# Performance work log

Hardware: AMD Instinct MI355X
Metric: run time of the kernel (lower is better)

Reference implementation:

```python
import jax, jax.numpy as jnp
import numpy as np

B, L, H = 512, 10, 256   # batch dialogs, max context len (=dia_len), hidden_size
D = 2 * H                # utt encoding dim (bidirectional)
E = 0.01                 # self.e
BN_EPS = 1e-5


def _linear(x, w, b):
    return x @ w.T + b


def _bn(x, g, b):
    # BatchNorm2d over channel dim 1 of [B, L, L, hid]; training-mode batch stats.
    m = jnp.mean(x, axis=(0, 2, 3), keepdims=True)
    v = jnp.mean((x - m) ** 2, axis=(0, 2, 3), keepdims=True)
    return (x - m) / jnp.sqrt(v + BN_EPS) * g[None, :, None, None] + b[None, :, None, None]


def setup_inputs() -> dict:
    key = jax.random.key(0)
    ks = jax.random.split(key, 24)
    u = lambda k, s: jax.random.uniform(k, s, jnp.float32, -0.02, 0.02)
    n = lambda k, s: jax.random.normal(k, s, jnp.float32) * 0.05
    inp = {
        'utt_encs': jax.random.normal(ks[0], (B, L, D), jnp.float32),
        'aij_eps': jax.random.normal(ks[1], (B, L, L), jnp.float32),
        'sij_eps': jax.random.normal(ks[2], (B, L, L), jnp.float32),
        'context_lens': jax.random.randint(ks[3], (B,), 2, L + 1),
        # mlp_aij_mij: Linear(4H->H), BN, ReLU, Linear(H->H), BN, ReLU, Linear(H->1)
        'a_w1': u(ks[4], (H, 2 * D)), 'a_b1': jnp.zeros((H,)),
        'a_g1': jnp.ones((L,)), 'a_be1': jnp.zeros((L,)),
        'a_w2': u(ks[5], (H, H)), 'a_b2': jnp.zeros((H,)),
        'a_g2': jnp.ones((L,)), 'a_be2': jnp.zeros((L,)),
        'a_w3': u(ks[6], (1, H)), 'a_b3': jnp.zeros((1,)),
        # mlp_sij: Linear(4H->H), BN, Tanh, Linear(H->H), BN, Tanh
        's_w1': u(ks[7], (H, 2 * D)), 's_b1': jnp.zeros((H,)),
        's_g1': jnp.ones((L,)), 's_be1': jnp.zeros((L,)),
        's_w2': u(ks[8], (H, H)), 's_b2': jnp.zeros((H,)),
        's_g2': jnp.ones((L,)), 's_be2': jnp.zeros((L,)),
        'mu_w': u(ks[9], (1, H)), 'mu_b': jnp.zeros((1,)),
        'sg_w': u(ks[10], (1, H)), 'sg_b': jnp.zeros((1,)),
        # update_hidden_state: GRU(2H -> H), single step
        'gru_wi': n(ks[11], (3 * H, D)), 'gru_wh': n(ks[12], (3 * H, H)),
        'gru_bi': jnp.zeros((3 * H,)), 'gru_bh': jnp.zeros((3 * H,)),
    }
    return inp


def reference(utt_encs, aij_eps, sij_eps, context_lens,
              a_w1, a_b1, a_g1, a_be1, a_w2, a_b2, a_g2, a_be2, a_w3, a_b3,
              s_w1, s_b1, s_g1, s_be1, s_w2, s_b2, s_g2, s_be2,
              mu_w, mu_b, sg_w, sg_b, gru_wi, gru_wh, gru_bi, gru_bh):
    # pairwise concat [B, L, L, 4H]
    x_ij = jnp.concatenate([
        jnp.broadcast_to(utt_encs[:, :, None, :], (B, L, L, D)),
        jnp.broadcast_to(utt_encs[:, None, :, :], (B, L, L, D)),
    ], axis=-1)
    # aij branch
    h1 = jax.nn.relu(_bn(_linear(x_ij, a_w1, a_b1), a_g1, a_be1))
    h2 = jax.nn.relu(_bn(_linear(h1, a_w2, a_b2), a_g2, a_be2))
    aij_mij = _linear(h2, a_w3, a_b3)[..., 0]                      # [B, L, L]
    aij_mu = jax.nn.softplus(aij_mij) + E
    aij_std = jnp.sqrt(jax.nn.softplus((1.0 - aij_mu) * aij_mu) + E)
    aij = jax.nn.softplus(aij_eps * aij_std + aij_mu) + E
    # sij branch
    t1 = jnp.tanh(_bn(_linear(x_ij, s_w1, s_b1), s_g1, s_be1))
    sij_latent = jnp.tanh(_bn(_linear(t1, s_w2, s_b2), s_g2, s_be2))
    sij_mu = _linear(sij_latent, mu_w, mu_b)[..., 0]
    sij_sigma = _linear(sij_latent, sg_w, sg_b)[..., 0]
    sij = sij_eps * jnp.sqrt(aij * sij_sigma * sij_sigma) + aij * sij_mu
    wij = aij * sij                                                # [B, L, L]
    # per-dialog aggregation (vectorized): anchor = context_lens - 1,
    # neighbors are j < anchor (anchor row, anchor excluded, j <= num_neighbours)
    anchor = context_lens - 1                                      # [B]
    w_row = jnp.take_along_axis(wij, anchor[:, None, None], axis=1)[:, 0, :]  # [B, L]
    mask = jnp.arange(L)[None, :] < anchor[:, None]
    logits = jnp.where(mask, w_row, -jnp.inf)
    p = jax.nn.softmax(logits, axis=-1)
    p = jnp.where(mask, p, 0.0)
    message = jnp.einsum('bj,bjd->bd', p, utt_encs)                # [B, 2H]
    ue_a = jnp.take_along_axis(utt_encs, anchor[:, None, None], axis=1)[:, 0, :]
    h0 = ue_a[:, :H] + ue_a[:, H:]                                 # [B, H]
    # single GRU step (torch GRU cell math)
    gi = message @ gru_wi.T + gru_bi
    gh = h0 @ gru_wh.T + gru_bh
    i_r, i_z, i_n = jnp.split(gi, 3, axis=-1)
    h_r, h_z, h_n = jnp.split(gh, 3, axis=-1)
    r = jax.nn.sigmoid(i_r + h_r)
    z = jax.nn.sigmoid(i_z + h_z)
    ncand = jnp.tanh(i_n + r * h_n)
    return (1.0 - z) * ncand + z * h0                              # [B, H]
```

## Files before the change

kernel.cpp:

```cpp
#include <hip/hip_runtime.h>
#include <math.h>


typedef __attribute__((ext_vector_type(8))) short short8;
typedef __attribute__((ext_vector_type(4))) float f32x4;

__device__ __forceinline__ float softplusf(float x) {
  return x > 0.f ? x + log1pf(expf(-x)) : log1pf(expf(x));
}
__device__ __forceinline__ float wred64(float v) {
#pragma unroll
  for (int o = 32; o > 0; o >>= 1) v += __shfl_down(v, o);
  return v;
}
__device__ __forceinline__ unsigned short f2bf(float f) {
  unsigned int u = __float_as_uint(f);
  u += 0x7fffu + ((u >> 16) & 1u);
  return (unsigned short)(u >> 16);
}
__device__ __forceinline__ float bf2f(unsigned short u) {
  return __uint_as_float(((unsigned int)u) << 16);
}
__device__ __forceinline__ float tanh_fast(float x) {
  float ex = __expf(2.f * x);
  return 1.f - 2.f / (ex + 1.f);
}
__device__ __forceinline__ float sigmoid_fast(float x) {
  return 1.f / (1.f + __expf(-x));
}
__device__ __forceinline__ short8 pack8(const float* __restrict__ p) {
  float4 v0 = *(const float4*)p;
  float4 v1 = *(const float4*)(p + 4);
  short8 r;
  r[0] = (short)f2bf(v0.x); r[1] = (short)f2bf(v0.y);
  r[2] = (short)f2bf(v0.z); r[3] = (short)f2bf(v0.w);
  r[4] = (short)f2bf(v1.x); r[5] = (short)f2bf(v1.y);
  r[6] = (short)f2bf(v1.z); r[7] = (short)f2bf(v1.w);
  return r;
}

__global__ __launch_bounds__(256) void prep_weights(
    const float* __restrict__ utt,
    const float* __restrict__ a_w1, const float* __restrict__ s_w1,
    const float* __restrict__ a_w2, const float* __restrict__ s_w2,
    const float* __restrict__ gru_wi, const float* __restrict__ gru_wh,
    unsigned short* __restrict__ Af, unsigned short* __restrict__ Bf,
    unsigned short* __restrict__ W2fa, unsigned short* __restrict__ W2fs,
    unsigned short* __restrict__ wibf, unsigned short* __restrict__ whbf) {
  int i = blockIdx.x * 256 + threadIdx.x;
  if (i < 327680) {
    int lane = i & 63, ks = (i >> 6) & 15, rb = i >> 10;
    int row = rb * 16 + (lane & 15);
    int k = ks * 32 + (lane >> 4) * 8;
    *(short8*)&Af[i * 8] = pack8(&utt[row * 512 + k]);
    return;
  }
  i -= 327680;
  if (i < 65536) {
    int lane = i & 63, cf = (i >> 6) & 3, ks = (i >> 8) & 15, cb = i >> 12;
    int c = cb * 64 + cf * 16 + (lane & 15);
    int k = ks * 32 + (lane >> 4) * 8;
    const float* src;
    if (c < 256)       src = &a_w1[c * 1024 + k];
    else if (c < 512)  src = &a_w1[(c - 256) * 1024 + 512 + k];
    else if (c < 768)  src = &s_w1[(c - 512) * 1024 + k];
    else               src = &s_w1[(c - 768) * 1024 + 512 + k];
    *(short8*)&Bf[i * 8] = pack8(src);
    return;
  }
  i -= 65536;
  if (i < 8192) {
    int lane = i & 63, cf = (i >> 6) & 3, ks = (i >> 8) & 7, cb = i >> 11;
    int c = cb * 64 + cf * 16 + (lane & 15);
    int k = ks * 32 + (lane >> 4) * 8;
    *(short8*)&W2fa[i * 8] = pack8(&a_w2[c * 256 + k]);
    return;
  }
  i -= 8192;
  if (i < 8192) {
    int lane = i & 63, cf = (i >> 6) & 3, ks = (i >> 8) & 7, cb = i >> 11;
    int c = cb * 64 + cf * 16 + (lane & 15);
    int k = ks * 32 + (lane >> 4) * 8;
    *(short8*)&W2fs[i * 8] = pack8(&s_w2[c * 256 + k]);
    return;
  }
  i -= 8192;
  if (i < 49152) { *(short8*)&wibf[i * 8] = pack8(&gru_wi[i * 8]); return; }
  i -= 49152;
  *(short8*)&whbf[i * 8] = pack8(&gru_wh[i * 8]);
}

__global__ __launch_bounds__(256) void gemm_pq_swz(
    const unsigned short* __restrict__ Af, const unsigned short* __restrict__ Bf,
    unsigned short* __restrict__ C) {
  int t = threadIdx.x;
  int w = t >> 6, l = t & 63, li = l & 15, lg = l >> 4;
  int rb0 = blockIdx.x * 4;
  int cb = blockIdx.y * 4 + w;
  const unsigned short* Bb = Bf + cb * (16 * 4 * 512);
  f32x4 acc[4][4] = {};
  short8 acur[4], bcur[4], anxt[4], bnxt[4];
#pragma unroll
  for (int fr = 0; fr < 4; ++fr) acur[fr] = *(const short8*)&Af[((rb0 + fr) * 16 + 0) * 512 + l * 8];
#pragma unroll
  for (int cf = 0; cf < 4; ++cf) bcur[cf] = *(const short8*)&Bb[(0 * 4 + cf) * 512 + l * 8];
  for (int ks = 0; ks < 16; ++ks) {
    if (ks < 15) {
#pragma unroll
      for (int fr = 0; fr < 4; ++fr) anxt[fr] = *(const short8*)&Af[((rb0 + fr) * 16 + ks + 1) * 512 + l * 8];
#pragma unroll
      for (int cf = 0; cf < 4; ++cf) bnxt[cf] = *(const short8*)&Bb[((ks + 1) * 4 + cf) * 512 + l * 8];
    }
#pragma unroll
    for (int fr = 0; fr < 4; ++fr)
#pragma unroll
      for (int cf = 0; cf < 4; ++cf)
        acc[fr][cf] = __builtin_amdgcn_mfma_f32_16x16x32_bf16(acur[fr], bcur[cf], acc[fr][cf], 0, 0, 0);
#pragma unroll
    for (int fr = 0; fr < 4; ++fr) acur[fr] = anxt[fr];
#pragma unroll
    for (int cf = 0; cf < 4; ++cf) bcur[cf] = bnxt[cf];
  }
  int rowBase = blockIdx.x * 64, colBase = cb * 64;
#pragma unroll
  for (int fr = 0; fr < 4; ++fr)
#pragma unroll
    for (int reg = 0; reg < 4; ++reg) {
      int r = rowBase + fr * 16 + lg * 4 + reg;
      unsigned short* crow = C + r * 1024 + colBase + li;
#pragma unroll
      for (int cf = 0; cf < 4; ++cf) crow[cf * 16] = f2bf(acc[fr][cf][reg]);
    }
}

__global__ __launch_bounds__(256) void stats_kernel(
    const unsigned short* __restrict__ PQ, const float* __restrict__ a_b1,
    const float* __restrict__ s_b1, float* __restrict__ Part) {
  __shared__ float lbins[4][32];
  int b = blockIdx.x, t = threadIdx.x;
  int w = t >> 6, l = t & 63;
  int half = t >> 7;
  int tt = t & 127;
  int c0 = tt * 2;
  int p_off = half ? 512 : 0;
  const unsigned short* base = PQ + b * 10240 + p_off;
  const float* b1 = half ? s_b1 : a_b1;
  float Q0[10], Q1[10];
#pragma unroll
  for (int j = 0; j < 10; ++j) {
    unsigned int qq = *(const unsigned int*)&base[j * 1024 + 256 + c0];
    Q0[j] = bf2f((unsigned short)qq);
    Q1[j] = bf2f((unsigned short)(qq >> 16));
  }
  float sq = 0.f, sq2 = 0.f, qb0 = 0.f, qb1 = 0.f;
#pragma unroll
  for (int j = 0; j < 10; ++j) {
    sq += Q0[j] + Q1[j];
    sq2 += Q0[j] * Q0[j] + Q1[j] * Q1[j];
    qb0 += Q0[j];
    qb1 += Q1[j];
  }
  qb0 *= 0.1f;
  qb1 *= 0.1f;
  float b10 = b1[c0], b11 = b1[c0 + 1];
  float r;
  r = wred64(sq);  if (l == 0) lbins[w][0] = r;
  r = wred64(sq2); if (l == 0) lbins[w][1] = r;
#pragma unroll
  for (int i = 0; i < 10; ++i) {
    unsigned int pp = *(const unsigned int*)&base[i * 1024 + c0];
    float P0 = bf2f((unsigned short)pp);
    float P1 = bf2f((unsigned short)(pp >> 16));
    float a0 = P0 + b10, a1 = P1 + b11;
    r = wred64(P0 + P1);                 if (l == 0) lbins[w][2 + i * 3] = r;
    r = wred64(a0 * a0 + a1 * a1);       if (l == 0) lbins[w][3 + i * 3] = r;
    r = wred64(a0 * qb0 + a1 * qb1);     if (l == 0) lbins[w][4 + i * 3] = r;
  }
  __syncthreads();
  if (t < 64) {
    int br = t >> 5, s = t & 31;
    Part[(b * 2 + br) * 32 + s] = lbins[br * 2][s] + lbins[br * 2 + 1][s];
  }
}

__global__ void reduce_bn1(const float* __restrict__ Part,
                           const float* __restrict__ a_b1, const float* __restrict__ s_b1,
                           const float* __restrict__ a_g1, const float* __restrict__ a_be1,
                           const float* __restrict__ s_g1, const float* __restrict__ s_be1,
                           float* __restrict__ ST) {
  __shared__ float tmp[256];
  __shared__ float mom[32];
  int br = blockIdx.x, t = threadIdx.x;
  int v = t & 31, c = t >> 5;
  float s = 0.f;
  for (int b = c * 64; b < c * 64 + 64; ++b) s += Part[(b * 2 + br) * 32 + v];
  tmp[t] = s;
  __syncthreads();
  if (t < 32) {
    float m = 0.f;
#pragma unroll
    for (int k = 0; k < 8; ++k) m += tmp[k * 32 + t];
    mom[t] = m;
  }
  __syncthreads();
  if (t < 10) {
    int i = t;
    const float* b1 = br ? s_b1 : a_b1;
    float bsum = 0.f;
    for (int h = 0; h < 256; ++h) bsum += b1[h];
    float meanb1 = bsum * (1.f / 256.f);
    const float invBH = 1.f / (512.f * 256.f);
    const float invBLH = 1.f / (512.f * 10.f * 256.f);
    float SP = mom[2 + i * 3], SA2 = mom[3 + i * 3], SPQ = mom[4 + i * 3];
    float SQ = mom[0], SQ2 = mom[1];
    float mean = SP * invBH + meanb1 + SQ * invBLH;
    float Ez2 = SA2 * invBH + 2.f * SPQ * invBH + SQ2 * invBLH;
    float var = Ez2 - mean * mean;
    float g = br ? s_g1[i] : a_g1[i];
    float be = br ? s_be1[i] : a_be1[i];
    float sc = g / sqrtf(var + 1e-5f);
    ST[64 + br * 20 + i] = sc;
    ST[64 + br * 20 + 10 + i] = be - mean * sc;
  }
}

__global__ __launch_bounds__(256, 4) void fused_layer2_half(
    const unsigned short* __restrict__ PQ, const float* __restrict__ ST,
    const float* __restrict__ a_b1, const float* __restrict__ s_b1,
    const unsigned short* __restrict__ W2fa, const unsigned short* __restrict__ W2fs,
    const float* __restrict__ a_b2, const float* __restrict__ s_b2,
    const int* __restrict__ cl, unsigned short* __restrict__ Z2a, unsigned short* __restrict__ Z2s,
    float* __restrict__ Part2) {
  __shared__ __align__(16) unsigned short Atile[64][264];
  __shared__ float bins[10];
  int b = blockIdx.x, half = blockIdx.y, br = blockIdx.z;
  int i0 = half * 5;
  int p_off = br ? 512 : 0;
  const float* b1 = br ? s_b1 : a_b1;
  const unsigned short* W2f = br ? W2fs : W2fa;
  const float* b2 = br ? s_b2 : a_b2;
  unsigned short* Z2out = br ? Z2s : Z2a;
  int sc_off = br ? 84 : 64;
  int t = threadIdx.x;
  int anc = cl[b] - 1;
  if (t < 10) bins[t] = 0.f;
  int w = t >> 6, l = t & 63, li = l & 15, lg = l >> 4;
  int colBase = w * 64;
  const unsigned short* Wb = W2f + w * (8 * 4 * 512);
  short8 bcur[4], bnxt[4];
#pragma unroll
  for (int cf = 0; cf < 4; ++cf) bcur[cf] = *(const short8*)&Wb[(0 * 4 + cf) * 512 + l * 8];
  float b2v[4];
#pragma unroll
  for (int cf = 0; cf < 4; ++cf) b2v[cf] = b2[colBase + cf * 16 + li];
  for (int idx = t; idx < 14 * 264; idx += 256) (&Atile[50][0])[idx] = 0;
  {
    int c = t;
    float b1c = b1[c];
    float P[5], Q[10];
#pragma unroll
    for (int j = 0; j < 10; ++j) Q[j] = bf2f(PQ[(b * 10 + j) * 1024 + p_off + 256 + c]);
#pragma unroll
    for (int il = 0; il < 5; ++il) P[il] = bf2f(PQ[(b * 10 + i0 + il) * 1024 + p_off + c]);
#pragma unroll
    for (int il = 0; il < 5; ++il) {
      float sc = ST[sc_off + i0 + il], sh = ST[sc_off + 10 + i0 + il];
      float base = (P[il] + b1c) * sc + sh;
#pragma unroll
      for (int j = 0; j < 10; ++j) {
        float z = base + Q[j] * sc;
        float h;
        if (br) {
          float ex = __expf(2.f * z);
          h = 1.f - 2.f / (ex + 1.f);
        } else {
          h = fmaxf(z, 0.f);
        }
        Atile[il * 10 + j][c] = f2bf(h);
      }
    }
  }
  __syncthreads();
  f32x4 acc[4][4] = {};
  for (int ks = 0; ks < 8; ++ks) {
    if (ks < 7) {
#pragma unroll
      for (int cf = 0; cf < 4; ++cf) bnxt[cf] = *(const short8*)&Wb[((ks + 1) * 4 + cf) * 512 + l * 8];
    }
    int ka = ks * 32 + lg * 8;
#pragma unroll
    for (int fr = 0; fr < 4; ++fr) {
      short8 afr = *(const short8*)&Atile[fr * 16 + li][ka];
#pragma unroll
      for (int cf = 0; cf < 4; ++cf)
        acc[fr][cf] = __builtin_amdgcn_mfma_f32_16x16x32_bf16(afr, bcur[cf], acc[fr][cf], 0, 0, 0);
    }
#pragma unroll
    for (int cf = 0; cf < 4; ++cf) bcur[cf] = bnxt[cf];
  }
#pragma unroll
  for (int fr = 0; fr < 4; ++fr) {
#pragma unroll
    for (int reg = 0; reg < 4; ++reg) {
      int row = fr * 16 + lg * 4 + reg;
      bool valid = row < 50;
      int il = row / 10, jj = row - il * 10;
      float z0 = acc[fr][0][reg] + b2v[0];
      float z1 = acc[fr][1][reg] + b2v[1];
      float z2 = acc[fr][2][reg] + b2v[2];
      float z3 = acc[fr][3][reg] + b2v[3];
      if (valid && (i0 + il) == anc) {
        unsigned short* dst = Z2out + (b * 10 + jj) * 256 + colBase + li;
        dst[0] = f2bf(z0); dst[16] = f2bf(z1); dst[32] = f2bf(z2); dst[48] = f2bf(z3);
      }
      float s = valid ? (z0 + z1 + z2 + z3) : 0.f;
      float q = valid ? (z0 * z0 + z1 * z1 + z2 * z2 + z3 * z3) : 0.f;
#pragma unroll
      for (int o = 1; o < 16; o <<= 1) {
        s += __shfl_xor(s, o);
        q += __shfl_xor(q, o);
      }
      if (li == 0 && valid) {
        atomicAdd(&bins[il], s);
        atomicAdd(&bins[5 + il], q);
      }
    }
  }
  __syncthreads();
  if (t < 5) {
    Part2[(br * 10 + i0 + t) * 512 + b] = bins[t];
    Part2[10240 + (br * 10 + i0 + t) * 512 + b] = bins[5 + t];
  }
}

__global__ __launch_bounds__(256) void gemm_gru2(
    const unsigned short* __restrict__ A0, const unsigned short* __restrict__ B0,
    float* __restrict__ C0, const float* __restrict__ bias0,
    const unsigned short* __restrict__ A1, const unsigned short* __restrict__ B1,
    float* __restrict__ C1, const float* __restrict__ bias1) {
  const unsigned short* A; const unsigned short* Bw; float* C; const float* bias; int K;
  if (blockIdx.z == 0) { A = A0; Bw = B0; C = C0; bias = bias0; K = 512; }
  else                 { A = A1; Bw = B1; C = C1; bias = bias1; K = 256; }
  int t = threadIdx.x;
  int w = t >> 6, l = t & 63, li = l & 15, lg = l >> 4;
  int rowBase = blockIdx.x * 32;
  int colBase = blockIdx.y * 256 + w * 64;
  f32x4 acc[2][4] = {};
  const unsigned short* Arow[2];
  const unsigned short* Brow[4];
#pragma unroll
  for (int fr = 0; fr < 2; ++fr) Arow[fr] = A + (rowBase + fr * 16 + li) * K;
#pragma unroll
  for (int cf = 0; cf < 4; ++cf) Brow[cf] = Bw + (colBase + cf * 16 + li) * K;
  for (int ks = 0; ks < K / 32; ++ks) {
    int ka = ks * 32 + lg * 8;
    short8 afr[2], bfr[4];
#pragma unroll
    for (int fr = 0; fr < 2; ++fr) afr[fr] = *(const short8*)&Arow[fr][ka];
#pragma unroll
    for (int cf = 0; cf < 4; ++cf) bfr[cf] = *(const short8*)&Brow[cf][ka];
#pragma unroll
    for (int fr = 0; fr < 2; ++fr)
#pragma unroll
      for (int cf = 0; cf < 4; ++cf)
        acc[fr][cf] = __builtin_amdgcn_mfma_f32_16x16x32_bf16(afr[fr], bfr[cf], acc[fr][cf], 0, 0, 0);
  }
  float b2v[4];
#pragma unroll
  for (int cf = 0; cf < 4; ++cf) b2v[cf] = bias[colBase + cf * 16 + li];
#pragma unroll
  for (int fr = 0; fr < 2; ++fr)
#pragma unroll
    for (int reg = 0; reg < 4; ++reg) {
      int r = rowBase + fr * 16 + lg * 4 + reg;
      float* crow = C + r * 768 + colBase + li;
#pragma unroll
      for (int cf = 0; cf < 4; ++cf) crow[cf * 16] = acc[fr][cf][reg] + b2v[cf];
    }
}

__global__ __launch_bounds__(256) void postproc_kernel(
    const float* __restrict__ Part2,
    const float* __restrict__ a_g2, const float* __restrict__ a_be2,
    const float* __restrict__ s_g2, const float* __restrict__ s_be2,
    const unsigned short* __restrict__ Z2a, const unsigned short* __restrict__ Z2s,
    const float* __restrict__ a_w3, const float* __restrict__ a_b3,
    const float* __restrict__ mu_w, const float* __restrict__ mu_b,
    const float* __restrict__ sg_w, const float* __restrict__ sg_b,
    const float* __restrict__ aij_eps, const float* __restrict__ sij_eps,
    const int* __restrict__ cl, const float* __restrict__ utt,
    unsigned short* __restrict__ msgbf, unsigned short* __restrict__ h0bf,
    float* __restrict__ h0out) {
  int b = blockIdx.x, t = threadIdx.x;
  int w = t >> 6, l = t & 63;
  int a = cl[b] - 1;
  __shared__ float bn2r[4];
  {
    int p = (w >> 1) * 10 + a;
    int off = (w & 1) ? 10240 : 0;
    float s = 0.f;
#pragma unroll
    for (int k = 0; k < 8; ++k) s += Part2[off + p * 512 + l + k * 64];
    s = wred64(s);
    if (l == 0) bn2r[w] = s;
  }
  __syncthreads();
  __shared__ float sc2[4];
  if (t < 2) {
    int br = t;
    const float invN = 1.f / (512.f * 10.f * 256.f);
    float m = bn2r[br * 2 + 0] * invN;
    float v = bn2r[br * 2 + 1] * invN - m * m;
    float g = br ? s_g2[a] : a_g2[a];
    float be = br ? s_be2[a] : a_be2[a];
    float sc = g / sqrtf(v + 1e-5f);
    sc2[br * 2] = sc;
    sc2[br * 2 + 1] = be - m * sc;
  }
  __syncthreads();
  float sc2a = sc2[0], sh2a = sc2[1], sc2s = sc2[2], sh2s = sc2[3];
  __shared__ float red[30];
#pragma unroll
  for (int m = 0; m < 3; ++m) {
    int j = w + 4 * m;
    if (j < 10) {
      float pa = 0.f, pm = 0.f, ps = 0.f;
#pragma unroll
      for (int cc = 0; cc < 4; ++cc) {
        int c = l + cc * 64;
        float za = bf2f(Z2a[(b * 10 + j) * 256 + c]);
        float va = fmaxf(za * sc2a + sh2a, 0.f);
        float zs = bf2f(Z2s[(b * 10 + j) * 256 + c]);
        float vs = tanh_fast(zs * sc2s + sh2s);
        pa += va * a_w3[c];
        pm += vs * mu_w[c];
        ps += vs * sg_w[c];
      }
      pa = wred64(pa); pm = wred64(pm); ps = wred64(ps);
      if (l == 0) { red[j] = pa; red[10 + j] = pm; red[20 + j] = ps; }
    }
  }
  __syncthreads();
  __shared__ float pw[10];
  __shared__ float wijs[16];
  if (t < 10) {
    int j = t;
    float amij = red[j] + a_b3[0];
    float amu = softplusf(amij) + 0.01f;
    float astd = sqrtf(softplusf((1.f - amu) * amu) + 0.01f);
    float ae = aij_eps[b * 100 + a * 10 + j];
    float aij = softplusf(ae * astd + amu) + 0.01f;
    float smu = red[10 + j] + mu_b[0];
    float ssg = red[20 + j] + sg_b[0];
    float se = sij_eps[b * 100 + a * 10 + j];
    float sij = se * sqrtf(aij * ssg * ssg) + aij * smu;
    wijs[j] = aij * sij;
  }
  __syncthreads();
  if (t == 0) {
    float mx = -1e30f;
    for (int j = 0; j < a; ++j) mx = fmaxf(mx, wijs[j]);
    float e[10];
    float den = 0.f;
    for (int j = 0; j < a; ++j) { e[j] = expf(wijs[j] - mx); den += e[j]; }
    for (int j = 0; j < 10; ++j) pw[j] = (j < a) ? e[j] / den : 0.f;
  }
  __syncthreads();
#pragma unroll
  for (int dd = 0; dd < 2; ++dd) {
    int d = t + dd * 256;
    float mv = 0.f;
#pragma unroll
    for (int j = 0; j < 10; ++j) mv += pw[j] * utt[(b * 10 + j) * 512 + d];
    msgbf[b * 512 + d] = f2bf(mv);
  }
  float u1 = utt[(b * 10 + a) * 512 + t];
  float u2 = utt[(b * 10 + a) * 512 + 256 + t];
  float h0v = u1 + u2;
  h0out[b * 256 + t] = h0v;
  h0bf[b * 256 + t] = f2bf(h0v);
}

__global__ __launch_bounds__(256) void gru_final(const float* __restrict__ gi,
                                                 const float* __restrict__ gh,
                                                 const float* __restrict__ h0,
                                                 float* __restrict__ out) {
  int idx = blockIdx.x * 256 + threadIdx.x;
  int b = idx >> 8, h = idx & 255;
  float ir = gi[b * 768 + h], iz = gi[b * 768 + 256 + h], inn = gi[b * 768 + 512 + h];
  float hr = gh[b * 768 + h], hz = gh[b * 768 + 256 + h], hn = gh[b * 768 + 512 + h];
  float r = sigmoid_fast(ir + hr);
  float z = sigmoid_fast(iz + hz);
  float n = tanh_fast(inn + r * hn);
  out[idx] = (1.f - z) * n + z * h0[b * 256 + h];
}

extern "C" void kernel_launch(void* const* d_in, const int* in_sizes, int n_in,
                              void* d_out, int out_size, void* d_ws, size_t ws_size,
                              hipStream_t stream) {
  const float* utt = (const float*)d_in[0];
  const float* aij_eps = (const float*)d_in[1];
  const float* sij_eps = (const float*)d_in[2];
  const int* cl = (const int*)d_in[3];
  const float* a_w1 = (const float*)d_in[4];
  const float* a_b1 = (const float*)d_in[5];
  const float* a_g1 = (const float*)d_in[6];
  const float* a_be1 = (const float*)d_in[7];
  const float* a_w2 = (const float*)d_in[8];
  const float* a_b2 = (const float*)d_in[9];
  const float* a_g2 = (const float*)d_in[10];
  const float* a_be2 = (const float*)d_in[11];
  const float* a_w3 = (const float*)d_in[12];
  const float* a_b3 = (const float*)d_in[13];
  const float* s_w1 = (const float*)d_in[14];
  const float* s_b1 = (const float*)d_in[15];
  const float* s_g1 = (const float*)d_in[16];
  const float* s_be1 = (const float*)d_in[17];
  const float* s_w2 = (const float*)d_in[18];
  const float* s_b2 = (const float*)d_in[19];
  const float* s_g2 = (const float*)d_in[20];
  const float* s_be2 = (const float*)d_in[21];
  const float* mu_w = (const float*)d_in[22];
  const float* mu_b = (const float*)d_in[23];
  const float* sg_w = (const float*)d_in[24];
  const float* sg_b = (const float*)d_in[25];
  const float* gru_wi = (const float*)d_in[26];
  const float* gru_wh = (const float*)d_in[27];
  const float* gru_bi = (const float*)d_in[28];
  const float* gru_bh = (const float*)d_in[29];

  float* ws = (float*)d_ws;
  float* ST = ws;
  unsigned short* Af = (unsigned short*)(ws + 256);
  unsigned short* Bf = Af + 2621440;
  unsigned short* W2fa = Bf + 524288;
  unsigned short* W2fs = W2fa + 65536;
  unsigned short* wibf = W2fs + 65536;
  unsigned short* whbf = wibf + 393216;
  float* PQf = (float*)(whbf + 196608);
  unsigned short* PQ = (unsigned short*)PQf;
  unsigned short* Z2a = (unsigned short*)(PQf + 5242880);
  unsigned short* Z2s = Z2a + 1310720;
  float* Part = PQf + 5242880 + 1310720;
  float* Part2 = Part + 32768;
  float* tailf = PQf + 2621440;
  unsigned short* msgbf = (unsigned short*)tailf;
  unsigned short* h0bf = msgbf + 262144;
  float* h0 = tailf + 196608;
  float* gi = tailf + 327680;
  float* gh = gi + 393216;

  prep_weights<<<1888, 256, 0, stream>>>(utt, a_w1, s_w1, a_w2, s_w2, gru_wi, gru_wh,
                                         Af, Bf, W2fa, W2fs, wibf, whbf);
  gemm_pq_swz<<<dim3(80, 4), 256, 0, stream>>>(Af, Bf, PQ);
  stats_kernel<<<512, 256, 0, stream>>>(PQ, a_b1, s_b1, Part);
  reduce_bn1<<<2, 256, 0, stream>>>(Part, a_b1, s_b1, a_g1, a_be1, s_g1, s_be1, ST);
  fused_layer2_half<<<dim3(512, 2, 2), 256, 0, stream>>>(PQ, ST, a_b1, s_b1, W2fa, W2fs,
                                                         a_b2, s_b2, cl, Z2a, Z2s, Part2);
  postproc_kernel<<<512, 256, 0, stream>>>(Part2, a_g2, a_be2, s_g2, s_be2,
                                           Z2a, Z2s, a_w3, a_b3, mu_w, mu_b, sg_w, sg_b,
                                           aij_eps, sij_eps, cl, utt, msgbf, h0bf, h0);
  gemm_gru2<<<dim3(16, 3, 2), 256, 0, stream>>>(msgbf, wibf, gi, gru_bi,
                                                h0bf, whbf, gh, gru_bh);
  gru_final<<<512, 256, 0, stream>>>(gi, gh, h0, (float*)d_out);
}
```

Measured before the change: 113.1 us.

## Fuse utt bf16 conversion into GEMM and fold BN1 reduce into stats

The GEMM now reads fp32 utterance encodings directly and converts them to bf16 in registers. This removes the separate pre-swizzled Af buffer and the write and read it costs in prep_weights. The reduce_bn1 kernel is removed: the last stats block, found with an atomic counter that prep_weights resets, does the final BN1 reduction, saving one launch. Softmax uses __expf. In exchange the GEMM reads twice as many A bytes in fp32, and the final reduction runs serially on a single block.

```diff
diff --git a/kernel.cpp b/kernel.cpp
--- a/kernel.cpp
+++ b/kernel.cpp
@@ -38,24 +38,25 @@
   r[6] = (short)f2bf(v1.z); r[7] = (short)f2bf(v1.w);
   return r;
 }
+__device__ __forceinline__ short8 cvt8(float4 v0, float4 v1) {
+  short8 r;
+  r[0] = (short)f2bf(v0.x); r[1] = (short)f2bf(v0.y);
+  r[2] = (short)f2bf(v0.z); r[3] = (short)f2bf(v0.w);
+  r[4] = (short)f2bf(v1.x); r[5] = (short)f2bf(v1.y);
+  r[6] = (short)f2bf(v1.z); r[7] = (short)f2bf(v1.w);
+  return r;
+}
 
 __global__ __launch_bounds__(256) void prep_weights(
-    const float* __restrict__ utt,
     const float* __restrict__ a_w1, const float* __restrict__ s_w1,
     const float* __restrict__ a_w2, const float* __restrict__ s_w2,
     const float* __restrict__ gru_wi, const float* __restrict__ gru_wh,
-    unsigned short* __restrict__ Af, unsigned short* __restrict__ Bf,
+    unsigned short* __restrict__ Bf,
     unsigned short* __restrict__ W2fa, unsigned short* __restrict__ W2fs,
-    unsigned short* __restrict__ wibf, unsigned short* __restrict__ whbf) {
+    unsigned short* __restrict__ wibf, unsigned short* __restrict__ whbf,
+    unsigned int* __restrict__ Cnt) {
+  if (blockIdx.x == 0 && threadIdx.x == 0) *Cnt = 0;
   int i = blockIdx.x * 256 + threadIdx.x;
-  if (i < 327680) {
-    int lane = i & 63, ks = (i >> 6) & 15, rb = i >> 10;
-    int row = rb * 16 + (lane & 15);
-    int k = ks * 32 + (lane >> 4) * 8;
-    *(short8*)&Af[i * 8] = pack8(&utt[row * 512 + k]);
-    return;
-  }
-  i -= 327680;
   if (i < 65536) {
     int lane = i & 63, cf = (i >> 6) & 3, ks = (i >> 8) & 15, cb = i >> 12;
     int c = cb * 64 + cf * 16 + (lane & 15);
@@ -87,11 +88,11 @@
   i -= 8192;
   if (i < 49152) { *(short8*)&wibf[i * 8] = pack8(&gru_wi[i * 8]); return; }
   i -= 49152;
-  *(short8*)&whbf[i * 8] = pack8(&gru_wh[i * 8]);
+  if (i < 24576) *(short8*)&whbf[i * 8] = pack8(&gru_wh[i * 8]);
 }
 
 __global__ __launch_bounds__(256) void gemm_pq_swz(
-    const unsigned short* __restrict__ Af, const unsigned short* __restrict__ Bf,
+    const float* __restrict__ utt, const unsigned short* __restrict__ Bf,
     unsigned short* __restrict__ C) {
   int t = threadIdx.x;
   int w = t >> 6, l = t & 63, li = l & 15, lg = l >> 4;
@@ -99,15 +100,27 @@
   int cb = blockIdx.y * 4 + w;
   const unsigned short* Bb = Bf + cb * (16 * 4 * 512);
   f32x4 acc[4][4] = {};
-  short8 acur[4], bcur[4], anxt[4], bnxt[4];
-#pragma unroll
-  for (int fr = 0; fr < 4; ++fr) acur[fr] = *(const short8*)&Af[((rb0 + fr) * 16 + 0) * 512 + l * 8];
+  short8 acur[4], bcur[4], bnxt[4];
+  float4 araw0[4], araw1[4];
+  const float* Arow[4];
+#pragma unroll
+  for (int fr = 0; fr < 4; ++fr) Arow[fr] = utt + ((rb0 + fr) * 16 + li) * 512 + lg * 8;
+#pragma unroll
+  for (int fr = 0; fr < 4; ++fr) {
+    araw0[fr] = *(const float4*)&Arow[fr][0];
+    araw1[fr] = *(const float4*)&Arow[fr][4];
+  }
 #pragma unroll
   for (int cf = 0; cf < 4; ++cf) bcur[cf] = *(const short8*)&Bb[(0 * 4 + cf) * 512 + l * 8];
+#pragma unroll
+  for (int fr = 0; fr < 4; ++fr) acur[fr] = cvt8(araw0[fr], araw1[fr]);
   for (int ks = 0; ks < 16; ++ks) {
     if (ks < 15) {
 #pragma unroll
-      for (int fr = 0; fr < 4; ++fr) anxt[fr] = *(const short8*)&Af[((rb0 + fr) * 16 + ks + 1) * 512 + l * 8];
+      for (int fr = 0; fr < 4; ++fr) {
+        araw0[fr] = *(const float4*)&Arow[fr][(ks + 1) * 32];
+        araw1[fr] = *(const float4*)&Arow[fr][(ks + 1) * 32 + 4];
+      }
 #pragma unroll
       for (int cf = 0; cf < 4; ++cf) bnxt[cf] = *(const short8*)&Bb[((ks + 1) * 4 + cf) * 512 + l * 8];
     }
@@ -116,10 +129,12 @@
 #pragma unroll
       for (int cf = 0; cf < 4; ++cf)
         acc[fr][cf] = __builtin_amdgcn_mfma_f32_16x16x32_bf16(acur[fr], bcur[cf], acc[fr][cf], 0, 0, 0);
-#pragma unroll
-    for (int fr = 0; fr < 4; ++fr) acur[fr] = anxt[fr];
-#pragma unroll
-    for (int cf = 0; cf < 4; ++cf) bcur[cf] = bnxt[cf];
+    if (ks < 15) {
+#pragma unroll
+      for (int fr = 0; fr < 4; ++fr) acur[fr] = cvt8(araw0[fr], araw1[fr]);
+#pragma unroll
+      for (int cf = 0; cf < 4; ++cf) bcur[cf] = bnxt[cf];
+    }
   }
   int rowBase = blockIdx.x * 64, colBase = cb * 64;
 #pragma unroll
@@ -135,7 +150,10 @@
 
 __global__ __launch_bounds__(256) void stats_kernel(
     const unsigned short* __restrict__ PQ, const float* __restrict__ a_b1,
-    const float* __restrict__ s_b1, float* __restrict__ Part) {
+    const float* __restrict__ s_b1,
+    const float* __restrict__ a_g1, const float* __restrict__ a_be1,
+    const float* __restrict__ s_g1, const float* __restrict__ s_be1,
+    float* __restrict__ Part, float* __restrict__ ST, unsigned int* __restrict__ Cnt) {
   __shared__ float lbins[4][32];
   int b = blockIdx.x, t = threadIdx.x;
   int w = t >> 6, l = t & 63;
@@ -144,7 +162,7 @@
   int c0 = tt * 2;
   int p_off = half ? 512 : 0;
   const unsigned short* base = PQ + b * 10240 + p_off;
-  const float* b1 = half ? s_b1 : a_b1;
+  const float* b1h = half ? s_b1 : a_b1;
   float Q0[10], Q1[10];
 #pragma unroll
   for (int j = 0; j < 10; ++j) {
@@ -162,7 +180,7 @@
   }
   qb0 *= 0.1f;
   qb1 *= 0.1f;
-  float b10 = b1[c0], b11 = b1[c0 + 1];
+  float b10 = b1h[c0], b11 = b1h[c0 + 1];
   float r;
   r = wred64(sq);  if (l == 0) lbins[w][0] = r;
   r = wred64(sq2); if (l == 0) lbins[w][1] = r;
@@ -181,46 +199,48 @@
     int br = t >> 5, s = t & 31;
     Part[(b * 2 + br) * 32 + s] = lbins[br * 2][s] + lbins[br * 2 + 1][s];
   }
-}
-
-__global__ void reduce_bn1(const float* __restrict__ Part,
-                           const float* __restrict__ a_b1, const float* __restrict__ s_b1,
-                           const float* __restrict__ a_g1, const float* __restrict__ a_be1,
-                           const float* __restrict__ s_g1, const float* __restrict__ s_be1,
-                           float* __restrict__ ST) {
+  __threadfence();
+  __syncthreads();
+  __shared__ int isLast;
+  if (t == 0) isLast = (atomicAdd(Cnt, 1u) == 511u) ? 1 : 0;
+  __syncthreads();
+  if (!isLast) return;
+  __threadfence();
   __shared__ float tmp[256];
   __shared__ float mom[32];
-  int br = blockIdx.x, t = threadIdx.x;
-  int v = t & 31, c = t >> 5;
-  float s = 0.f;
-  for (int b = c * 64; b < c * 64 + 64; ++b) s += Part[(b * 2 + br) * 32 + v];
-  tmp[t] = s;
-  __syncthreads();
-  if (t < 32) {
-    float m = 0.f;
-#pragma unroll
-    for (int k = 0; k < 8; ++k) m += tmp[k * 32 + t];
-    mom[t] = m;
-  }
-  __syncthreads();
-  if (t < 10) {
-    int i = t;
-    const float* b1 = br ? s_b1 : a_b1;
-    float bsum = 0.f;
-    for (int h = 0; h < 256; ++h) bsum += b1[h];
-    float meanb1 = bsum * (1.f / 256.f);
-    const float invBH = 1.f / (512.f * 256.f);
-    const float invBLH = 1.f / (512.f * 10.f * 256.f);
-    float SP = mom[2 + i * 3], SA2 = mom[3 + i * 3], SPQ = mom[4 + i * 3];
-    float SQ = mom[0], SQ2 = mom[1];
-    float mean = SP * invBH + meanb1 + SQ * invBLH;
-    float Ez2 = SA2 * invBH + 2.f * SPQ * invBH + SQ2 * invBLH;
-    float var = Ez2 - mean * mean;
-    float g = br ? s_g1[i] : a_g1[i];
-    float be = br ? s_be1[i] : a_be1[i];
-    float sc = g / sqrtf(var + 1e-5f);
-    ST[64 + br * 20 + i] = sc;
-    ST[64 + br * 20 + 10 + i] = be - mean * sc;
+  for (int br = 0; br < 2; ++br) {
+    int v = t & 31, c = t >> 5;
+    float s = 0.f;
+    for (int bb = c * 64; bb < c * 64 + 64; ++bb) s += Part[(bb * 2 + br) * 32 + v];
+    tmp[t] = s;
+    __syncthreads();
+    if (t < 32) {
+      float m = 0.f;
+#pragma unroll
+      for (int k = 0; k < 8; ++k) m += tmp[k * 32 + t];
+      mom[t] = m;
+    }
+    __syncthreads();
+    if (t < 10) {
+      int i = t;
+      const float* b1 = br ? s_b1 : a_b1;
+      float bsum = 0.f;
+      for (int h = 0; h < 256; ++h) bsum += b1[h];
+      float meanb1 = bsum * (1.f / 256.f);
+      const float invBH = 1.f / (512.f * 256.f);
+      const float invBLH = 1.f / (512.f * 10.f * 256.f);
+      float SP = mom[2 + i * 3], SA2 = mom[3 + i * 3], SPQ = mom[4 + i * 3];
+      float SQ = mom[0], SQ2 = mom[1];
+      float mean = SP * invBH + meanb1 + SQ * invBLH;
+      float Ez2 = SA2 * invBH + 2.f * SPQ * invBH + SQ2 * invBLH;
+      float var = Ez2 - mean * mean;
+      float g = br ? s_g1[i] : a_g1[i];
+      float be = br ? s_be1[i] : a_be1[i];
+      float sc = g / sqrtf(var + 1e-5f);
+      ST[64 + br * 20 + i] = sc;
+      ST[64 + br * 20 + 10 + i] = be - mean * sc;
+    }
+    __syncthreads();
   }
 }
 
@@ -462,7 +482,7 @@
     for (int j = 0; j < a; ++j) mx = fmaxf(mx, wijs[j]);
     float e[10];
     float den = 0.f;
-    for (int j = 0; j < a; ++j) { e[j] = expf(wijs[j] - mx); den += e[j]; }
+    for (int j = 0; j < a; ++j) { e[j] = __expf(wijs[j] - mx); den += e[j]; }
     for (int j = 0; j < 10; ++j) pw[j] = (j < a) ? e[j] / den : 0.f;
   }
   __syncthreads();
@@ -531,8 +551,8 @@
 
   float* ws = (float*)d_ws;
   float* ST = ws;
-  unsigned short* Af = (unsigned short*)(ws + 256);
-  unsigned short* Bf = Af + 2621440;
+  unsigned short* Af_unused = (unsigned short*)(ws + 256);
+  unsigned short* Bf = Af_unused + 2621440;
   unsigned short* W2fa = Bf + 524288;
   unsigned short* W2fs = W2fa + 65536;
   unsigned short* wibf = W2fs + 65536;
@@ -543,6 +563,7 @@
   unsigned short* Z2s = Z2a + 1310720;
   float* Part = PQf + 5242880 + 1310720;
   float* Part2 = Part + 32768;
+  unsigned int* Cnt = (unsigned int*)(Part2 + 20480);
   float* tailf = PQf + 2621440;
   unsigned short* msgbf = (unsigned short*)tailf;
   unsigned short* h0bf = msgbf + 262144;
@@ -550,11 +571,11 @@
   float* gi = tailf + 327680;
   float* gh = gi + 393216;
 
-  prep_weights<<<1888, 256, 0, stream>>>(utt, a_w1, s_w1, a_w2, s_w2, gru_wi, gru_wh,
-                                         Af, Bf, W2fa, W2fs, wibf, whbf);
-  gemm_pq_swz<<<dim3(80, 4), 256, 0, stream>>>(Af, Bf, PQ);
-  stats_kernel<<<512, 256, 0, stream>>>(PQ, a_b1, s_b1, Part);
-  reduce_bn1<<<2, 256, 0, stream>>>(Part, a_b1, s_b1, a_g1, a_be1, s_g1, s_be1, ST);
+  prep_weights<<<608, 256, 0, stream>>>(a_w1, s_w1, a_w2, s_w2, gru_wi, gru_wh,
+                                        Bf, W2fa, W2fs, wibf, whbf, Cnt);
+  gemm_pq_swz<<<dim3(80, 4), 256, 0, stream>>>(utt, Bf, PQ);
+  stats_kernel<<<512, 256, 0, stream>>>(PQ, a_b1, s_b1, a_g1, a_be1, s_g1, s_be1,
+                                        Part, ST, Cnt);
   fused_layer2_half<<<dim3(512, 2, 2), 256, 0, stream>>>(PQ, ST, a_b1, s_b1, W2fa, W2fs,
                                                          a_b2, s_b2, cl, Z2a, Z2s, Part2);
   postproc_kernel<<<512, 256, 0, stream>>>(Part2, a_g2, a_be2, s_g2, s_be2,
```

Result: slower. 154.1 us (+36.2%).
